# Kernel tuning notes

Hardware: AMD Instinct MI355X
Metric: run time of the kernel (lower is better)

The kernel has to match this reference:

```python
import jax, jax.numpy as jnp
import numpy as np

N, M, D = 16384, 16384, 16
MAX_NORM = 0.7  # keep points strictly inside Poincare ball

def _to_ball(v):
    # rescale so every point has norm < MAX_NORM
    n = jnp.linalg.norm(v, axis=1, keepdims=True)
    return MAX_NORM * v / (1.0 + n)

def setup_inputs() -> dict:
    key = jax.random.key(0)
    k1, k2 = jax.random.split(key)
    set1 = _to_ball(jax.random.normal(k1, (N, D), dtype=jnp.float32))
    set2 = _to_ball(jax.random.normal(k2, (M, D), dtype=jnp.float32))
    return {"set1": set1, "set2": set2}

def hypcdist(x, y, epsilon=0.0):
    # ||x_i - y_j||^2 for all pairs: [N, M]
    diff = x[:, None, :] - y[None, :, :]
    sqdist = jnp.sum(diff * diff, axis=-1)
    x_norm = jnp.sum(x * x, axis=1)[:, None]   # [N,1]
    y_norm = jnp.sum(y * y, axis=1)[None, :]   # [1,M]
    u = 1.0 + 2.0 * sqdist / ((1.0 - x_norm) * (1.0 - y_norm)) + epsilon
    v = jnp.sqrt(u * u - 1.0)
    return jnp.log(u + v)  # arcosh(u)

def reference(set1, set2):
    d2 = hypcdist(set1, set2)                 # [N, M]
    term_1 = jnp.mean(jnp.min(d2, axis=1))    # for each point in set1, nearest in set2
    term_2 = jnp.mean(jnp.min(d2, axis=0))    # for each point in set2, nearest in set1
    return term_1 + term_2                    # directed=False
```

## Files before the change

### kernel.cpp

```cpp
#include <hip/hip_runtime.h>
#include <math.h>

#define NPTS 16384
#define DIM  16
#define KH   64
#define CSPLIT 8
#define COLS_PER_BLOCK (NPTS / CSPLIT)
#define CHUNK_COLS 256
#define NCHUNK (COLS_PER_BLOCK / CHUNK_COLS)
#define JT_PER_CHUNK (CHUNK_COLS / 16)
#define ROWS_PER_BLOCK 512
#define RBLK (NPTS / ROWS_PER_BLOCK)
#define MT 8

typedef _Float16 f16x8 __attribute__((ext_vector_type(8)));
typedef float    f32x4 __attribute__((ext_vector_type(4)));

__global__ __launch_bounds__(256) void prep_kernel(const float* __restrict__ s1,
                                                   const float* __restrict__ s2,
                                                   _Float16* __restrict__ Xp,
                                                   _Float16* __restrict__ Yp,
                                                   unsigned int* __restrict__ rowfinal,
                                                   float* __restrict__ out) {
    int b = blockIdx.x, tid = threadIdx.x;
    int idx = b * 256 + tid;
    rowfinal[idx] = 0xFFFFFFFFu;
    if (idx == 0) out[0] = 0.f;

    int isX = (b < 64);
    const float* src = isX ? s1 : s2;
    _Float16* dst = isX ? Xp : Yp;
    int p = (isX ? b : b - 64) * 256 + tid;

    const float4* s4 = (const float4*)(src + (size_t)p * DIM);
    float4 A = s4[0], B = s4[1], C = s4[2], D = s4[3];
    float v[DIM] = {A.x,A.y,A.z,A.w, B.x,B.y,B.z,B.w,
                    C.x,C.y,C.z,C.w, D.x,D.y,D.z,D.w};
    float n2 = 0.f;
#pragma unroll
    for (int k = 0; k < DIM; ++k) n2 = fmaf(v[k], v[k], n2);
    float r = 1.0f / (1.0f - n2);
    float a[18];
#pragma unroll
    for (int k = 0; k < DIM; ++k) a[k] = r * v[k];
    if (isX) { a[16] = -0.5f * r * n2; a[17] = r; }
    else     { a[16] = r;              a[17] = -0.5f * r * n2; }

    __attribute__((aligned(16))) _Float16 buf[KH];
#pragma unroll
    for (int k = 0; k < 18; ++k) {
        _Float16 hi = (_Float16)a[k];
        _Float16 lo = (_Float16)(a[k] - (float)hi);
        if (isX) { buf[k] = hi; buf[18 + k] = lo; buf[36 + k] = hi; }
        else     { buf[k] = hi; buf[18 + k] = hi; buf[36 + k] = lo; }
    }
#pragma unroll
    for (int k = 54; k < KH; ++k) buf[k] = (_Float16)0.f;

    int g = p >> 4, c = p & 15;
    const uint4* b4 = (const uint4*)buf;
#pragma unroll
    for (int sq = 0; sq < 8; ++sq) {
        size_t off = (size_t)g * 1024 + (size_t)(sq >> 2) * 512 + (size_t)(sq & 3) * 128 + (size_t)c * 8;
        *(uint4*)(dst + off) = b4[sq];
    }
}

__global__ __launch_bounds__(256, 2) void pairs_kernel(const _Float16* __restrict__ Xp,
                                                       const _Float16* __restrict__ Yp,
                                                       unsigned int* __restrict__ rowfinal) {
    __shared__ __align__(16) _Float16 Bs[CHUNK_COLS * KH];

    const int b = blockIdx.x;
    const int pass = b >> 8;
    const int within = b & 255;
    const int r  = within >> 3;
    const int cs = within & 7;

    const _Float16* Aset = pass ? Yp : Xp;
    const _Float16* Bset = pass ? Xp : Yp;
    unsigned int* outMin = rowfinal + pass * NPTS;

    const int tid = threadIdx.x;
    const int lane = tid & 63, w = tid >> 6;
    const int c = lane & 15, quad = lane >> 4;

    f16x8 af[MT][2];
#pragma unroll
    for (int t = 0; t < MT; ++t) {
        int g = r * 32 + w * 8 + t;
        af[t][0] = *(const f16x8*)&Aset[(size_t)g * 1024 + (size_t)lane * 8];
        af[t][1] = *(const f16x8*)&Aset[(size_t)g * 1024 + 512 + (size_t)lane * 8];
    }

    f32x4 rowmax[MT];
#pragma unroll
    for (int t = 0; t < MT; ++t)
        rowmax[t] = (f32x4){-INFINITY, -INFINITY, -INFINITY, -INFINITY};

    const char* Bbase = (const char*)Bset + (size_t)cs * ((size_t)COLS_PER_BLOCK * KH * 2);

    for (int ch = 0; ch < NCHUNK; ++ch) {
        const char* gsrc = Bbase + (size_t)ch * (CHUNK_COLS * KH * 2) + (size_t)tid * 16;
        char* lb = (char*)Bs + (size_t)tid * 16;
#pragma unroll
        for (int e = 0; e < 8; ++e) {
            __builtin_amdgcn_global_load_lds(
                (const __attribute__((address_space(1))) unsigned int*)(gsrc + e * 4096),
                (__attribute__((address_space(3))) unsigned int*)(lb + e * 4096),
                16, 0, 0);
        }
        __syncthreads();

#pragma unroll 4
        for (int jt = 0; jt < JT_PER_CHUNK; ++jt) {
            f16x8 bf0 = *(const f16x8*)&Bs[jt * 1024 + lane * 8];
            f16x8 bf1 = *(const f16x8*)&Bs[jt * 1024 + 512 + lane * 8];
#pragma unroll
            for (int t = 0; t < MT; ++t) {
                f32x4 acc = (f32x4){0.f, 0.f, 0.f, 0.f};
                acc = __builtin_amdgcn_mfma_f32_16x16x32_f16(af[t][0], bf0, acc, 0, 0, 0);
                acc = __builtin_amdgcn_mfma_f32_16x16x32_f16(af[t][1], bf1, acc, 0, 0, 0);
                rowmax[t][0] = fmaxf(rowmax[t][0], acc[0]);
                rowmax[t][1] = fmaxf(rowmax[t][1], acc[1]);
                rowmax[t][2] = fmaxf(rowmax[t][2], acc[2]);
                rowmax[t][3] = fmaxf(rowmax[t][3], acc[3]);
            }
        }
        __syncthreads();
    }

#pragma unroll
    for (int t = 0; t < MT; ++t) {
#pragma unroll
        for (int e = 0; e < 4; ++e) {
            float m = rowmax[t][e];
            m = fmaxf(m, __shfl_xor(m, 1, 64));
            m = fmaxf(m, __shfl_xor(m, 2, 64));
            m = fmaxf(m, __shfl_xor(m, 4, 64));
            m = fmaxf(m, __shfl_xor(m, 8, 64));
            if (c == 0) {
                int row = r * 512 + w * 128 + t * 16 + quad * 4 + e;
                atomicMin(&outMin[row], __float_as_uint(m));
            }
        }
    }
}

__global__ __launch_bounds__(256) void finalize_kernel(const unsigned int* __restrict__ rowfinal,
                                                       float* __restrict__ out) {
    int idx = blockIdx.x * 256 + threadIdx.x;
    float f = __uint_as_float(rowfinal[idx]);
    float t = -4.0f * f;
    float d = log1pf(t + sqrtf(t * (t + 2.0f)));
    float val = d * (1.0f / NPTS);

    __shared__ float sred[256];
    sred[threadIdx.x] = val;
    __syncthreads();
    for (int s = 128; s > 0; s >>= 1) {
        if (threadIdx.x < s) sred[threadIdx.x] += sred[threadIdx.x + s];
        __syncthreads();
    }
    if (threadIdx.x == 0) atomicAdd(out, sred[0]);
}

extern "C" void kernel_launch(void* const* d_in, const int* in_sizes, int n_in,
                              void* d_out, int out_size, void* d_ws, size_t ws_size,
                              hipStream_t stream) {
    const float* set1 = (const float*)d_in[0];
    const float* set2 = (const float*)d_in[1];
    float* out = (float*)d_out;

    _Float16* Xp = (_Float16*)d_ws;
    _Float16* Yp = Xp + (size_t)NPTS * KH;
    unsigned int* rowfinal = (unsigned int*)(Yp + (size_t)NPTS * KH);

    prep_kernel<<<128, 256, 0, stream>>>(set1, set2, Xp, Yp, rowfinal, out);
    pairs_kernel<<<2 * RBLK * CSPLIT, 256, 0, stream>>>(Xp, Yp, rowfinal);
    finalize_kernel<<<2 * NPTS / 256, 256, 0, stream>>>(rowfinal, out);
}
```

Measured before the change: 115.5 us.

## Drop fp16 hi/lo split to single MFMA, fuse finalize via last-block reduction

Each coordinate is now stored as a single fp16 value instead of a hi/lo split, so K shrinks from 64 to 32. That halves the MFMA count and the LDS and global traffic per pair. The column split doubles and occupancy is raised to 4 blocks per CU. The finalize kernel is removed: the last block to finish, found through an atomic counter, computes arcosh and the mean. Dropping the split-precision correction lowers the accuracy of the min-distance values, which could matter for the tolerance check.

```diff
diff --git a/kernel.cpp b/kernel.cpp
--- a/kernel.cpp
+++ b/kernel.cpp
@@ -3,8 +3,8 @@
 
 #define NPTS 16384
 #define DIM  16
-#define KH   64
-#define CSPLIT 8
+#define KH   32
+#define CSPLIT 16
 #define COLS_PER_BLOCK (NPTS / CSPLIT)
 #define CHUNK_COLS 256
 #define NCHUNK (COLS_PER_BLOCK / CHUNK_COLS)
@@ -12,6 +12,7 @@
 #define ROWS_PER_BLOCK 512
 #define RBLK (NPTS / ROWS_PER_BLOCK)
 #define MT 8
+#define NBLOCKS (2 * RBLK * CSPLIT)
 
 typedef _Float16 f16x8 __attribute__((ext_vector_type(8)));
 typedef float    f32x4 __attribute__((ext_vector_type(4)));
@@ -21,11 +22,11 @@
                                                    _Float16* __restrict__ Xp,
                                                    _Float16* __restrict__ Yp,
                                                    unsigned int* __restrict__ rowfinal,
-                                                   float* __restrict__ out) {
+                                                   unsigned int* __restrict__ counter) {
     int b = blockIdx.x, tid = threadIdx.x;
     int idx = b * 256 + tid;
     rowfinal[idx] = 0xFFFFFFFFu;
-    if (idx == 0) out[0] = 0.f;
+    if (idx == 0) *counter = 0u;
 
     int isX = (b < 64);
     const float* src = isX ? s1 : s2;
@@ -48,34 +49,31 @@
 
     __attribute__((aligned(16))) _Float16 buf[KH];
 #pragma unroll
-    for (int k = 0; k < 18; ++k) {
-        _Float16 hi = (_Float16)a[k];
-        _Float16 lo = (_Float16)(a[k] - (float)hi);
-        if (isX) { buf[k] = hi; buf[18 + k] = lo; buf[36 + k] = hi; }
-        else     { buf[k] = hi; buf[18 + k] = hi; buf[36 + k] = lo; }
-    }
+    for (int k = 0; k < 18; ++k) buf[k] = (_Float16)a[k];
 #pragma unroll
-    for (int k = 54; k < KH; ++k) buf[k] = (_Float16)0.f;
+    for (int k = 18; k < KH; ++k) buf[k] = (_Float16)0.f;
 
     int g = p >> 4, c = p & 15;
     const uint4* b4 = (const uint4*)buf;
 #pragma unroll
-    for (int sq = 0; sq < 8; ++sq) {
-        size_t off = (size_t)g * 1024 + (size_t)(sq >> 2) * 512 + (size_t)(sq & 3) * 128 + (size_t)c * 8;
-        *(uint4*)(dst + off) = b4[sq];
+    for (int q = 0; q < 4; ++q) {
+        size_t off = (size_t)g * 512 + (size_t)q * 128 + (size_t)c * 8;
+        *(uint4*)(dst + off) = b4[q];
     }
 }
 
-__global__ __launch_bounds__(256, 2) void pairs_kernel(const _Float16* __restrict__ Xp,
+__global__ __launch_bounds__(256, 4) void pairs_kernel(const _Float16* __restrict__ Xp,
                                                        const _Float16* __restrict__ Yp,
-                                                       unsigned int* __restrict__ rowfinal) {
+                                                       unsigned int* __restrict__ rowfinal,
+                                                       unsigned int* __restrict__ counter,
+                                                       float* __restrict__ out) {
     __shared__ __align__(16) _Float16 Bs[CHUNK_COLS * KH];
 
     const int b = blockIdx.x;
-    const int pass = b >> 8;
-    const int within = b & 255;
-    const int r  = within >> 3;
-    const int cs = within & 7;
+    const int pass = b >> 9;
+    const int within = b & 511;
+    const int r  = within >> 4;
+    const int cs = within & 15;
 
     const _Float16* Aset = pass ? Yp : Xp;
     const _Float16* Bset = pass ? Xp : Yp;
@@ -85,12 +83,11 @@
     const int lane = tid & 63, w = tid >> 6;
     const int c = lane & 15, quad = lane >> 4;
 
-    f16x8 af[MT][2];
+    f16x8 af[MT];
 #pragma unroll
     for (int t = 0; t < MT; ++t) {
         int g = r * 32 + w * 8 + t;
-        af[t][0] = *(const f16x8*)&Aset[(size_t)g * 1024 + (size_t)lane * 8];
-        af[t][1] = *(const f16x8*)&Aset[(size_t)g * 1024 + 512 + (size_t)lane * 8];
+        af[t] = *(const f16x8*)&Aset[(size_t)g * 512 + (size_t)lane * 8];
     }
 
     f32x4 rowmax[MT];
@@ -104,7 +101,7 @@
         const char* gsrc = Bbase + (size_t)ch * (CHUNK_COLS * KH * 2) + (size_t)tid * 16;
         char* lb = (char*)Bs + (size_t)tid * 16;
 #pragma unroll
-        for (int e = 0; e < 8; ++e) {
+        for (int e = 0; e < 4; ++e) {
             __builtin_amdgcn_global_load_lds(
                 (const __attribute__((address_space(1))) unsigned int*)(gsrc + e * 4096),
                 (__attribute__((address_space(3))) unsigned int*)(lb + e * 4096),
@@ -114,13 +111,11 @@
 
 #pragma unroll 4
         for (int jt = 0; jt < JT_PER_CHUNK; ++jt) {
-            f16x8 bf0 = *(const f16x8*)&Bs[jt * 1024 + lane * 8];
-            f16x8 bf1 = *(const f16x8*)&Bs[jt * 1024 + 512 + lane * 8];
+            f16x8 bf = *(const f16x8*)&Bs[jt * 512 + lane * 8];
 #pragma unroll
             for (int t = 0; t < MT; ++t) {
                 f32x4 acc = (f32x4){0.f, 0.f, 0.f, 0.f};
-                acc = __builtin_amdgcn_mfma_f32_16x16x32_f16(af[t][0], bf0, acc, 0, 0, 0);
-                acc = __builtin_amdgcn_mfma_f32_16x16x32_f16(af[t][1], bf1, acc, 0, 0, 0);
+                acc = __builtin_amdgcn_mfma_f32_16x16x32_f16(af[t], bf, acc, 0, 0, 0);
                 rowmax[t][0] = fmaxf(rowmax[t][0], acc[0]);
                 rowmax[t][1] = fmaxf(rowmax[t][1], acc[1]);
                 rowmax[t][2] = fmaxf(rowmax[t][2], acc[2]);
@@ -140,29 +135,39 @@
             m = fmaxf(m, __shfl_xor(m, 4, 64));
             m = fmaxf(m, __shfl_xor(m, 8, 64));
             if (c == 0) {
-                int row = r * 512 + w * 128 + t * 16 + quad * 4 + e;
+                int row = ((r * 32 + w * 8 + t) << 4) + quad * 4 + e;
                 atomicMin(&outMin[row], __float_as_uint(m));
             }
         }
     }
-}
 
-__global__ __launch_bounds__(256) void finalize_kernel(const unsigned int* __restrict__ rowfinal,
-                                                       float* __restrict__ out) {
-    int idx = blockIdx.x * 256 + threadIdx.x;
-    float f = __uint_as_float(rowfinal[idx]);
-    float t = -4.0f * f;
-    float d = log1pf(t + sqrtf(t * (t + 2.0f)));
-    float val = d * (1.0f / NPTS);
-
-    __shared__ float sred[256];
-    sred[threadIdx.x] = val;
+    __threadfence();
+    __shared__ int isLast;
+    if (tid == 0) {
+        unsigned int old = __hip_atomic_fetch_add(counter, 1u, __ATOMIC_ACQ_REL,
+                                                  __HIP_MEMORY_SCOPE_AGENT);
+        isLast = (old == NBLOCKS - 1);
+    }
     __syncthreads();
-    for (int s = 128; s > 0; s >>= 1) {
-        if (threadIdx.x < s) sred[threadIdx.x] += sred[threadIdx.x + s];
+    if (isLast) {
+        float sum = 0.f;
+        for (int k = 0; k < (2 * NPTS) / 256; ++k) {
+            int i = tid + k * 256;
+            unsigned int ub = __hip_atomic_load(&rowfinal[i], __ATOMIC_RELAXED,
+                                                __HIP_MEMORY_SCOPE_AGENT);
+            float f = __uint_as_float(ub);
+            float t = fmaxf(-4.0f * f, 0.0f);
+            sum += log1pf(t + sqrtf(t * (t + 2.0f)));
+        }
+        __shared__ float sred[256];
+        sred[tid] = sum;
         __syncthreads();
+        for (int s = 128; s > 0; s >>= 1) {
+            if (tid < s) sred[tid] += sred[tid + s];
+            __syncthreads();
+        }
+        if (tid == 0) out[0] = sred[0] * (1.0f / NPTS);
     }
-    if (threadIdx.x == 0) atomicAdd(out, sred[0]);
 }
 
 extern "C" void kernel_launch(void* const* d_in, const int* in_sizes, int n_in,
@@ -175,8 +180,8 @@
     _Float16* Xp = (_Float16*)d_ws;
     _Float16* Yp = Xp + (size_t)NPTS * KH;
     unsigned int* rowfinal = (unsigned int*)(Yp + (size_t)NPTS * KH);
+    unsigned int* counter = rowfinal + 2 * NPTS;
 
-    prep_kernel<<<128, 256, 0, stream>>>(set1, set2, Xp, Yp, rowfinal, out);
-    pairs_kernel<<<2 * RBLK * CSPLIT, 256, 0, stream>>>(Xp, Yp, rowfinal);
-    finalize_kernel<<<2 * NPTS / 256, 256, 0, stream>>>(rowfinal, out);
+    prep_kernel<<<128, 256, 0, stream>>>(set1, set2, Xp, Yp, rowfinal, counter);
+    pairs_kernel<<<NBLOCKS, 256, 0, stream>>>(Xp, Yp, rowfinal, counter, out);
 }
```

After: 218.4 us. 1.89x slower.
